# Kernel tuning notes

Hardware: AMD Instinct MI355X
Metric: run time of the kernel (lower is better)

The kernel has to match this reference:

```python
import jax, jax.numpy as jnp
import numpy as np

B, N, NC = 16, 25200, 80
CONF_THRES = 0.25
IOU_THRES = 0.45
MAX_DET = 300
MAX_WH = 7680.0   # yolov5 per-class box offset for class-aware NMS
TOPK = 1024       # pre-NMS candidate cap (fixed-shape stand-in for yolov5 max_nms)


def setup_inputs():
    key = jax.random.key(0)
    k1, k2 = jax.random.split(key)
    # xywh in pixel units (640x640 image, boxes up to ~120 px); obj/cls confidences in [0,1]
    xywh = jax.random.uniform(k1, (B, N, 4), dtype=jnp.float32) * jnp.array([640.0, 640.0, 120.0, 120.0], jnp.float32)
    conf = jax.random.uniform(k2, (B, N, 1 + NC), dtype=jnp.float32)
    return {"YOLOoutput": jnp.concatenate([xywh, conf], axis=-1)}


def _xywh2xyxy(x):
    cx, cy, w, h = x[..., 0], x[..., 1], x[..., 2], x[..., 3]
    return jnp.stack([cx - w / 2, cy - h / 2, cx + w / 2, cy + h / 2], axis=-1)


def _pairwise_iou(a, b):
    # a, b: [K,4] xyxy -> [K,K]
    lt = jnp.maximum(a[:, None, :2], b[None, :, :2])
    rb = jnp.minimum(a[:, None, 2:], b[None, :, 2:])
    wh = jnp.maximum(rb - lt, 0.0)
    inter = wh[..., 0] * wh[..., 1]
    area_a = (a[:, 2] - a[:, 0]) * (a[:, 3] - a[:, 1])
    area_b = (b[:, 2] - b[:, 0]) * (b[:, 3] - b[:, 1])
    return inter / (area_a[:, None] + area_b[None, :] - inter + 1e-7)


def _nms_single(pred):
    # pred: [N, 5+NC]
    obj = pred[:, 4]
    cls_conf = pred[:, 5:] * obj[:, None]      # conf = obj_conf * cls_conf (yolov5)
    conf = jnp.max(cls_conf, axis=-1)
    j = jnp.argmax(cls_conf, axis=-1)
    valid = (obj > CONF_THRES) & (conf > CONF_THRES)
    box = _xywh2xyxy(pred[:, :4])
    scores = jnp.where(valid, conf, -1.0)      # invalid candidates sink to bottom
    top_scores, idx = jax.lax.top_k(scores, TOPK)
    b = box[idx]                               # [TOPK,4]
    c = j[idx].astype(box.dtype)
    boxes_off = b + (c * MAX_WH)[:, None]      # class-aware NMS via per-class offset
    valid_k = top_scores > 0.0
    iou = _pairwise_iou(boxes_off, boxes_off)
    ar = jnp.arange(TOPK)

    def body(i, supp):
        active = jnp.logical_not(supp[i])
        return supp | (active & (iou[i] > IOU_THRES) & (ar > i))

    supp = jax.lax.fori_loop(0, TOPK, body, jnp.logical_not(valid_k))
    keep = valid_k & jnp.logical_not(supp)
    fs, fi = jax.lax.top_k(jnp.where(keep, top_scores, -1.0), MAX_DET)
    dv = fs > 0.0
    det_box = b[fi] * dv[:, None]              # zero out padded rows
    det = jnp.concatenate(
        [det_box, jnp.where(dv, fs, 0.0)[:, None], (c[fi] * dv)[:, None]], axis=-1
    )                                          # [MAX_DET, 6] = x1,y1,x2,y2,conf,cls
    return det, dv


def reference(YOLOoutput):
    det, dvalid = jax.vmap(_nms_single)(YOLOoutput)   # [B,MAX_DET,6], [B,MAX_DET]
    scores = det[..., 4]
    mean_conf = jnp.max(scores, axis=1)               # = 0 when image has no detections
    n = dvalid.sum(axis=1)
    terms = jnp.abs(det[..., 0:2] - det[..., 2:4]) * scores[..., None]  # padded rows are 0
    s = terms.sum(axis=(1, 2))
    wh = jnp.where(n > 0, s / (2.0 * jnp.maximum(n, 1)), 0.0)  # mean over n*2 elements
    conf_addition = mean_conf.sum() / B
    w_and_h = wh.sum() / B
    return conf_addition, w_and_h, det[2]
```

## Files before the change

kernel.cpp:

```cpp
#include <hip/hip_runtime.h>
#include <hip/hip_bf16.h>

typedef unsigned long long u64;
typedef unsigned int u32;

#define BATCH 16
#define NANCH 25200
#define NCLS 80
#define NFEAT 85
#define TOPK 1024
#define MAXDET 300
#define CONF_T 0.25f
#define IOU_T 0.45f
#define MAX_WH 7680.0f

#define TILE_A 64

__device__ __forceinline__ void gload_lds16(const void* g, void* l) {
    __builtin_amdgcn_global_load_lds(
        (const __attribute__((address_space(1))) unsigned int*)g,
        (__attribute__((address_space(3))) unsigned int*)l, 16, 0, 0);
}

__global__ __launch_bounds__(256) void score_kernel(const float* __restrict__ in,
                                                    u64* __restrict__ keys) {
    __shared__ float ld[TILE_A * NFEAT];
    const int b = blockIdx.y, tid = threadIdx.x;
    const int wv = tid >> 6, lane = tid & 63;
    const int a0 = blockIdx.x * TILE_A;
    const int na = min(TILE_A, NANCH - a0);
    const int nbytes = na * NFEAT * 4;
    const char* gbase = (const char*)(in + ((size_t)b * NANCH + a0) * NFEAT);
#pragma unroll
    for (int r = 0; r < 6; ++r) {
        const int off = (r * 4 + wv) << 10;
        const int myb = off + lane * 16;
        if (myb < nbytes)
            gload_lds16(gbase + myb, (char*)ld + off);
    }
    __syncthreads();
    const int a = tid >> 2, q = tid & 3;
    if (a < na) {
        const float* p = ld + a * NFEAT;
        float obj = p[4];
        float best = -1e30f;
        int bj = 0;
#pragma unroll
        for (int k = 0; k < 20; ++k) {
            float v = p[5 + q * 20 + k] * obj;
            if (v > best) { best = v; bj = q * 20 + k; }
        }
#pragma unroll
        for (int d = 1; d < 4; d <<= 1) {
            float ob = __shfl_xor(best, d, 64);
            int oj = __shfl_xor(bj, d, 64);
            if (ob > best || (ob == best && oj < bj)) { best = ob; bj = oj; }
        }
        if (q == 0) {
            bool valid = (obj > CONF_T) && (best > CONF_T);
            float sc = valid ? best : -1.0f;
            u32 sb = __float_as_uint(sc);
            u32 ord = sb ^ ((sb & 0x80000000u) ? 0xFFFFFFFFu : 0x80000000u);
            int idx = a0 + a;
            keys[(size_t)b * NANCH + idx] =
                ((u64)ord << 32) | ((u64)((u32)(idx ^ 0xFFFF) & 0xFFFFu) << 8) | (u64)bj;
        }
    }
}

__global__ __launch_bounds__(1024) void select_topk(const u64* __restrict__ keys,
                                                    const float* __restrict__ in,
                                                    float4* __restrict__ box4,
                                                    float4* __restrict__ boxoff4,
                                                    float* __restrict__ score,
                                                    float* __restrict__ cls,
                                                    u64* __restrict__ vmask,
                                                    float* __restrict__ out) {
    const int b = blockIdx.x, tid = threadIdx.x;
    const int lane = tid & 63, wv = tid >> 6;
    const u64* kb = keys + (size_t)b * NANCH;
    __shared__ u32 hist[4096];
    __shared__ u32 wtot[16];
    __shared__ u32 wsfx[16];
    __shared__ u32 s_prefix12, s_cnt;
    __shared__ u64 buf[2048];

    if (b == 0 && tid == 0) { out[0] = 0.0f; out[1] = 0.0f; }

#pragma unroll
    for (int i = 0; i < 4; ++i) hist[tid * 4 + i] = 0u;
    __syncthreads();
#pragma unroll 4
    for (int n = tid; n < NANCH; n += 1024) {
        u32 hi = (u32)(kb[n] >> 32);
        atomicAdd(&hist[hi >> 20], 1u);
    }
    __syncthreads();
    u32 h0 = hist[tid * 4], h1 = hist[tid * 4 + 1];
    u32 h2 = hist[tid * 4 + 2], h3 = hist[tid * 4 + 3];
    u32 s3v = h3, s2v = h2 + s3v, s1v = h1 + s2v, s0v = h0 + s1v;
    u32 S = s0v;
#pragma unroll
    for (int d = 1; d < 64; d <<= 1) {
        u32 o = __shfl_down(S, d, 64);
        if (lane + d < 64) S += o;
    }
    if (lane == 0) wtot[wv] = S;
    __syncthreads();
    if (tid == 0) {
        u32 acc = 0;
        for (int w = 15; w >= 0; --w) { wsfx[w] = acc; acc += wtot[w]; }
    }
    __syncthreads();
    {
        const u32 E = wsfx[wv] + (S - s0v);
        const u32 v0 = E + s0v, v1 = E + s1v, v2 = E + s2v, v3 = E + s3v, v4 = E;
        if (v0 >= (u32)TOPK && v1 < (u32)TOPK) s_prefix12 = (u32)(tid * 4 + 0);
        if (v1 >= (u32)TOPK && v2 < (u32)TOPK) s_prefix12 = (u32)(tid * 4 + 1);
        if (v2 >= (u32)TOPK && v3 < (u32)TOPK) s_prefix12 = (u32)(tid * 4 + 2);
        if (v3 >= (u32)TOPK && v4 < (u32)TOPK) s_prefix12 = (u32)(tid * 4 + 3);
    }
    if (tid == 0) s_cnt = 0u;
    __syncthreads();
    const u32 p12 = s_prefix12;
#pragma unroll 4
    for (int n = tid; n < NANCH; n += 1024) {
        u64 k = kb[n];
        if (((u32)(k >> 32) >> 20) > p12) {
            u32 pos = atomicAdd(&s_cnt, 1u);
            if (pos < 2048u) buf[pos] = k;
        }
    }
    __syncthreads();
#pragma unroll 4
    for (int n = tid; n < NANCH; n += 1024) {
        u64 k = kb[n];
        if (((u32)(k >> 32) >> 20) == p12) {
            u32 pos = atomicAdd(&s_cnt, 1u);
            if (pos < 2048u) buf[pos] = k;
        }
    }
    __syncthreads();
    u32 cnt = s_cnt; if (cnt > 2048u) cnt = 2048u;
    for (int n = (int)cnt + tid; n < 2048; n += 1024) buf[n] = 0ull;
    __syncthreads();

    const int base = wv * 128;
    u64 r0 = buf[base + lane], r1 = buf[base + 64 + lane];
    for (int k2 = 2; k2 <= 128; k2 <<= 1) {
        const bool d0 = (((base + lane) & k2) == 0);
        const bool d1 = (((base + 64 + lane) & k2) == 0);
        for (int jj = (k2 >> 1); jj >= 1; jj >>= 1) {
            if (jj == 64) {
                u64 mx = r0 > r1 ? r0 : r1, mn = r0 > r1 ? r1 : r0;
                r0 = d0 ? mx : mn; r1 = d0 ? mn : mx;
            } else {
                const bool up = (lane & jj) != 0;
                u64 v0 = __shfl_xor(r0, jj, 64);
                u64 v1 = __shfl_xor(r1, jj, 64);
                const bool km0 = (d0 != up), km1 = (d1 != up);
                r0 = km0 ? (r0 > v0 ? r0 : v0) : (r0 < v0 ? r0 : v0);
                r1 = km1 ? (r1 > v1 ? r1 : v1) : (r1 < v1 ? r1 : v1);
            }
        }
    }
    for (int k2 = 256; k2 <= 2048; k2 <<= 1) {
        buf[base + lane] = r0; buf[base + 64 + lane] = r1;
        __syncthreads();
        for (int jj = (k2 >> 1); jj >= 128; jj >>= 1) {
            int i = ((tid & ~(jj - 1)) << 1) | (tid & (jj - 1));
            int part = i | jj;
            u64 a = buf[i], c = buf[part];
            bool sw = ((i & k2) == 0) ? (a < c) : (a > c);
            if (sw) { buf[i] = c; buf[part] = a; }
            __syncthreads();
        }
        r0 = buf[base + lane]; r1 = buf[base + 64 + lane];
        const bool d0 = (((base + lane) & k2) == 0);
        for (int jj = 64; jj >= 1; jj >>= 1) {
            if (jj == 64) {
                u64 mx = r0 > r1 ? r0 : r1, mn = r0 > r1 ? r1 : r0;
                r0 = d0 ? mx : mn; r1 = d0 ? mn : mx;
            } else {
                const bool up = (lane & jj) != 0;
                u64 v0 = __shfl_xor(r0, jj, 64);
                u64 v1 = __shfl_xor(r1, jj, 64);
                const bool km = (d0 != up);
                r0 = km ? (r0 > v0 ? r0 : v0) : (r0 < v0 ? r0 : v0);
                r1 = km ? (r1 > v1 ? r1 : v1) : (r1 < v1 ? r1 : v1);
            }
        }
    }
    buf[base + lane] = r0; buf[base + 64 + lane] = r1;
    __syncthreads();

    u64 k = buf[tid];
    u32 ord = (u32)(k >> 32);
    u32 sb = (ord & 0x80000000u) ? (ord ^ 0x80000000u) : ~ord;
    float sc = __uint_as_float(sb);
    int idx = (int)((((u32)(k >> 8)) & 0xFFFFu) ^ 0xFFFFu);
    int j = (int)(k & 0xFFu);
    const float* pr = in + ((size_t)b * NANCH + idx) * NFEAT;
    float cx = pr[0], cy = pr[1], ww = pr[2], hh = pr[3];
    float x1 = cx - ww / 2.0f, y1 = cy - hh / 2.0f;
    float x2 = cx + ww / 2.0f, y2 = cy + hh / 2.0f;
    float c = (float)j;
    float cm = c * MAX_WH;
    box4[b * TOPK + tid]    = make_float4(x1, y1, x2, y2);
    boxoff4[b * TOPK + tid] = make_float4(x1 + cm, y1 + cm, x2 + cm, y2 + cm);
    score[b * TOPK + tid] = sc;
    cls[b * TOPK + tid] = c;
    u64 bal = __ballot(sc > 0.0f);
    if ((tid & 63) == 0) vmask[b * 16 + (tid >> 6)] = bal;
}

__global__ __launch_bounds__(256) void iou_mask(const float4* __restrict__ boxoff4,
                                                u64* __restrict__ M) {
    __shared__ float4 sbx[TOPK];
    const int b = blockIdx.x >> 8;
    const int rb = blockIdx.x & 255;
    const int i = (rb << 2) | (threadIdx.x >> 6);
    const int lane = threadIdx.x & 63;
    const int tw = rb >> 4;
    const int jmin = tw << 6;
    for (int t = jmin + threadIdx.x; t < TOPK; t += 256) sbx[t] = boxoff4[b * TOPK + t];
    __syncthreads();
    const float4 A = sbx[i];
    const float areaA = (A.z - A.x) * (A.w - A.y);
    u64 myword = 0ull;
#pragma unroll 4
    for (int t = tw; t < 16; ++t) {
        int j = (t << 6) | lane;
        float4 Bx = sbx[j];
        float lx = fmaxf(A.x, Bx.x), ly = fmaxf(A.y, Bx.y);
        float rx = fminf(A.z, Bx.z), ry = fminf(A.w, Bx.w);
        float iw = fmaxf(rx - lx, 0.0f), ih = fmaxf(ry - ly, 0.0f);
        float inter = iw * ih;
        float areaB = (Bx.z - Bx.x) * (Bx.w - Bx.y);
        float iou = inter / (areaA + areaB - inter + 1e-7f);
        bool pred = (iou > IOU_T) && (j > i);
        u64 bal = __ballot(pred);
        if (lane == t) myword = bal;
    }
    if (lane < 16) M[((size_t)b * TOPK + i) * 16 + lane] = myword;
}

__global__ __launch_bounds__(512) void nms_finalize(const u64* __restrict__ M,
                                                    const u64* __restrict__ vmask,
                                                    const float4* __restrict__ box4,
                                                    const float* __restrict__ score,
                                                    const float* __restrict__ cls,
                                                    float* __restrict__ out) {
    __shared__ u64 sM[TOPK * 16];
    __shared__ u64 kw[16];
    __shared__ int wpfx[17];
    __shared__ float sdet[MAXDET * 6];
    __shared__ float s_sum, s_max;
    const int b = blockIdx.x, tid = threadIdx.x;
    {
        const ulonglong2* Ms = (const ulonglong2*)(M + (size_t)b * TOPK * 16);
        ulonglong2* Ldst = (ulonglong2*)sM;
#pragma unroll 4
        for (int t = tid; t < TOPK * 8; t += 512) Ldst[t] = Ms[t];
    }
    for (int t = tid; t < MAXDET * 6; t += 512) sdet[t] = 0.0f;
    if (tid == 0) { s_sum = 0.0f; s_max = 0.0f; }
    __syncthreads();
    if (tid < 16) {
        const int w = tid;
        const u64 vm = vmask[b * 16 + w];
        u64 supp = ~vm;
        u64 rwA[16], rwB[16];
#pragma unroll
        for (int q = 0; q < 16; ++q) rwA[q] = sM[q * 16 + w];
        for (int wb = 0; wb < 16; ++wb) {
            u64 cur = __shfl(supp, wb, 64);
#pragma unroll
            for (int c4 = 0; c4 < 4; ++c4) {
                const int rn = wb * 64 + (c4 + 1) * 16;
                if (rn < 1024) {
#pragma unroll
                    for (int q = 0; q < 16; ++q) rwB[q] = sM[(rn + q) * 16 + w];
                }
                u64 rc[16];
#pragma unroll
                for (int q = 0; q < 16; ++q) rc[q] = __shfl(rwA[q], wb, 64);
                u64 ar0 = rc[0] | rc[4] | rc[8]  | rc[12];
                u64 ar1 = rc[1] | rc[5] | rc[9]  | rc[13];
                u64 ar2 = rc[2] | rc[6] | rc[10] | rc[14];
                u64 ar3 = rc[3] | rc[7] | rc[11] | rc[15];
                const u32 intra = (u32)(((ar0 | ar1) | (ar2 | ar3)) >> (c4 * 16)) & 0xFFFFu;
                const u32 actm  = (~(u32)(cur >> (c4 * 16))) & 0xFFFFu;
                if (intra == 0u || actm == 0u) {
                    u64 s0 = 0, s1 = 0, s2 = 0, s3 = 0;
                    u64 c0 = 0, c1 = 0, c2 = 0, c3 = 0;
#pragma unroll
                    for (int q = 0; q < 16; q += 4) {
                        const u64 m0 = ((actm >> (q + 0)) & 1u) ? ~0ull : 0ull;
                        const u64 m1 = ((actm >> (q + 1)) & 1u) ? ~0ull : 0ull;
                        const u64 m2 = ((actm >> (q + 2)) & 1u) ? ~0ull : 0ull;
                        const u64 m3 = ((actm >> (q + 3)) & 1u) ? ~0ull : 0ull;
                        s0 |= rwA[q + 0] & m0;  c0 |= rc[q + 0] & m0;
                        s1 |= rwA[q + 1] & m1;  c1 |= rc[q + 1] & m1;
                        s2 |= rwA[q + 2] & m2;  c2 |= rc[q + 2] & m2;
                        s3 |= rwA[q + 3] & m3;  c3 |= rc[q + 3] & m3;
                    }
                    supp |= (s0 | s1) | (s2 | s3);
                    cur  |= (c0 | c1) | (c2 | c3);
                } else {
#pragma unroll
                    for (int q = 0; q < 16; ++q) {
                        const int ii = c4 * 16 + q;
                        const bool act = ((cur >> ii) & 1ull) == 0ull;
                        supp = act ? (supp | rwA[q]) : supp;
                        cur  = act ? (cur  | rc[q])  : cur;
                    }
                }
#pragma unroll
                for (int q = 0; q < 16; ++q) rwA[q] = rwB[q];
            }
        }
        kw[w] = vm & ~supp;
    }
    __syncthreads();
    if (tid == 0) {
        int acc = 0;
        for (int w = 0; w < 16; ++w) { wpfx[w] = acc; acc += __popcll(kw[w]); }
        wpfx[16] = acc;
    }
    __syncthreads();
    for (int r = tid; r < TOPK; r += 512) {
        int w = r >> 6, bp = r & 63;
        if ((kw[w] >> bp) & 1ull) {
            int pos = wpfx[w] + __popcll(kw[w] & ((1ull << bp) - 1ull));
            if (pos < MAXDET) {
                float4 bx = box4[b * TOPK + r];
                float s = score[b * TOPK + r];
                float c = cls[b * TOPK + r];
                sdet[pos * 6 + 0] = bx.x;
                sdet[pos * 6 + 1] = bx.y;
                sdet[pos * 6 + 2] = bx.z;
                sdet[pos * 6 + 3] = bx.w;
                sdet[pos * 6 + 4] = s;
                sdet[pos * 6 + 5] = c;
                float term = (fabsf(bx.x - bx.z) + fabsf(bx.y - bx.w)) * s;
                atomicAdd(&s_sum, term);
                if (pos == 0) s_max = s;
            }
        }
    }
    __syncthreads();
    if (tid == 0) {
        int n = wpfx[16]; if (n > MAXDET) n = MAXDET;
        float wh = (n > 0) ? (s_sum / (2.0f * (float)n)) : 0.0f;
        atomicAdd(&out[0], s_max / (float)BATCH);
        atomicAdd(&out[1], wh / (float)BATCH);
    }
    if (b == 2) {
        for (int t = tid; t < MAXDET * 6; t += 512) out[2 + t] = sdet[t];
    }
}

extern "C" void kernel_launch(void* const* d_in, const int* in_sizes, int n_in,
                              void* d_out, int out_size, void* d_ws, size_t ws_size,
                              hipStream_t stream) {
    const float* in = (const float*)d_in[0];
    float* out = (float*)d_out;
    char* ws = (char*)d_ws;

    u64*    keys     = (u64*)   (ws + 0);
    float4* boxoff4  = (float4*)(ws + 3225600);
    float4* box4     = (float4*)(ws + 3487744);
    float*  score    = (float*) (ws + 3749888);
    float*  cls      = (float*) (ws + 3815424);
    u64*    vmask    = (u64*)   (ws + 3880960);
    u64*    M        = (u64*)   (ws + 3883008);

    score_kernel<<<dim3(394, BATCH), 256, 0, stream>>>(in, keys);
    select_topk<<<BATCH, 1024, 0, stream>>>(keys, in, box4, boxoff4, score, cls, vmask, out);
    iou_mask<<<BATCH * 256, 256, 0, stream>>>(boxoff4, M);
    nms_finalize<<<BATCH, 512, 0, stream>>>(M, vmask, box4, score, cls, out);
}
```

Before: 275.8 us.

## Fuse top-k selection, IoU mask and NMS finalize into one per-batch kernel

```diff
diff --git a/kernel.cpp b/kernel.cpp
--- a/kernel.cpp
+++ b/kernel.cpp
@@ -23,10 +23,12 @@
 }
 
 __global__ __launch_bounds__(256) void score_kernel(const float* __restrict__ in,
-                                                    u64* __restrict__ keys) {
+                                                    u64* __restrict__ keys,
+                                                    float* __restrict__ out) {
     __shared__ float ld[TILE_A * NFEAT];
     const int b = blockIdx.y, tid = threadIdx.x;
     const int wv = tid >> 6, lane = tid & 63;
+    if (blockIdx.x == 0 && b == 0 && tid == 0) { out[0] = 0.0f; out[1] = 0.0f; }
     const int a0 = blockIdx.x * TILE_A;
     const int na = min(TILE_A, NANCH - a0);
     const int nbytes = na * NFEAT * 4;
@@ -68,25 +70,31 @@
     }
 }
 
-__global__ __launch_bounds__(1024) void select_topk(const u64* __restrict__ keys,
+__global__ __launch_bounds__(1024) void fused_batch(const u64* __restrict__ keys,
                                                     const float* __restrict__ in,
-                                                    float4* __restrict__ box4,
-                                                    float4* __restrict__ boxoff4,
-                                                    float* __restrict__ score,
-                                                    float* __restrict__ cls,
-                                                    u64* __restrict__ vmask,
                                                     float* __restrict__ out) {
+    __shared__ u64 sM[TOPK * 16];
+    __shared__ float4 sbox[TOPK];
+    __shared__ float sscore[TOPK];
+    __shared__ unsigned char sclsa[TOPK];
+    __shared__ u64 kwv[16];
+    __shared__ u64 kw[16];
+    __shared__ int wpfx[17];
+    __shared__ u32 wtot[16];
+    __shared__ u32 wsfx[16];
+    __shared__ u32 s_prefix12, s_cnt;
+    __shared__ float s_sum, s_max;
+    u32* hist = (u32*)sM;
+    u64* buf  = sM + 2048;
+
     const int b = blockIdx.x, tid = threadIdx.x;
     const int lane = tid & 63, wv = tid >> 6;
     const u64* kb = keys + (size_t)b * NANCH;
-    __shared__ u32 hist[4096];
-    __shared__ u32 wtot[16];
-    __shared__ u32 wsfx[16];
-    __shared__ u32 s_prefix12, s_cnt;
-    __shared__ u64 buf[2048];
-
-    if (b == 0 && tid == 0) { out[0] = 0.0f; out[1] = 0.0f; }
-
+
+    if (b == 2) {
+        for (int t = tid; t < MAXDET * 6; t += 1024) out[2 + t] = 0.0f;
+    }
+    if (tid == 0) { s_sum = 0.0f; s_max = 0.0f; s_cnt = 0u; }
 #pragma unroll
     for (int i = 0; i < 4; ++i) hist[tid * 4 + i] = 0u;
     __syncthreads();
@@ -120,7 +128,6 @@
         if (v2 >= (u32)TOPK && v3 < (u32)TOPK) s_prefix12 = (u32)(tid * 4 + 2);
         if (v3 >= (u32)TOPK && v4 < (u32)TOPK) s_prefix12 = (u32)(tid * 4 + 3);
     }
-    if (tid == 0) s_cnt = 0u;
     __syncthreads();
     const u32 p12 = s_prefix12;
 #pragma unroll 4
@@ -145,130 +152,122 @@
     for (int n = (int)cnt + tid; n < 2048; n += 1024) buf[n] = 0ull;
     __syncthreads();
 
-    const int base = wv * 128;
-    u64 r0 = buf[base + lane], r1 = buf[base + 64 + lane];
-    for (int k2 = 2; k2 <= 128; k2 <<= 1) {
-        const bool d0 = (((base + lane) & k2) == 0);
-        const bool d1 = (((base + 64 + lane) & k2) == 0);
-        for (int jj = (k2 >> 1); jj >= 1; jj >>= 1) {
-            if (jj == 64) {
-                u64 mx = r0 > r1 ? r0 : r1, mn = r0 > r1 ? r1 : r0;
-                r0 = d0 ? mx : mn; r1 = d0 ? mn : mx;
-            } else {
-                const bool up = (lane & jj) != 0;
-                u64 v0 = __shfl_xor(r0, jj, 64);
-                u64 v1 = __shfl_xor(r1, jj, 64);
-                const bool km0 = (d0 != up), km1 = (d1 != up);
-                r0 = km0 ? (r0 > v0 ? r0 : v0) : (r0 < v0 ? r0 : v0);
-                r1 = km1 ? (r1 > v1 ? r1 : v1) : (r1 < v1 ? r1 : v1);
-            }
-        }
-    }
-    for (int k2 = 256; k2 <= 2048; k2 <<= 1) {
+    {
+        const int base = wv * 128;
+        u64 r0 = buf[base + lane], r1 = buf[base + 64 + lane];
+        for (int k2 = 2; k2 <= 128; k2 <<= 1) {
+            const bool d0 = (((base + lane) & k2) == 0);
+            const bool d1 = (((base + 64 + lane) & k2) == 0);
+            for (int jj = (k2 >> 1); jj >= 1; jj >>= 1) {
+                if (jj == 64) {
+                    u64 mx = r0 > r1 ? r0 : r1, mn = r0 > r1 ? r1 : r0;
+                    r0 = d0 ? mx : mn; r1 = d0 ? mn : mx;
+                } else {
+                    const bool up = (lane & jj) != 0;
+                    u64 v0 = __shfl_xor(r0, jj, 64);
+                    u64 v1 = __shfl_xor(r1, jj, 64);
+                    const bool km0 = (d0 != up), km1 = (d1 != up);
+                    r0 = km0 ? (r0 > v0 ? r0 : v0) : (r0 < v0 ? r0 : v0);
+                    r1 = km1 ? (r1 > v1 ? r1 : v1) : (r1 < v1 ? r1 : v1);
+                }
+            }
+        }
+        for (int k2 = 256; k2 <= 2048; k2 <<= 1) {
+            buf[base + lane] = r0; buf[base + 64 + lane] = r1;
+            __syncthreads();
+            for (int jj = (k2 >> 1); jj >= 128; jj >>= 1) {
+                int i = ((tid & ~(jj - 1)) << 1) | (tid & (jj - 1));
+                int part = i | jj;
+                u64 a = buf[i], c = buf[part];
+                bool sw = ((i & k2) == 0) ? (a < c) : (a > c);
+                if (sw) { buf[i] = c; buf[part] = a; }
+                __syncthreads();
+            }
+            r0 = buf[base + lane]; r1 = buf[base + 64 + lane];
+            const bool d0 = (((base + lane) & k2) == 0);
+            for (int jj = 64; jj >= 1; jj >>= 1) {
+                if (jj == 64) {
+                    u64 mx = r0 > r1 ? r0 : r1, mn = r0 > r1 ? r1 : r0;
+                    r0 = d0 ? mx : mn; r1 = d0 ? mn : mx;
+                } else {
+                    const bool up = (lane & jj) != 0;
+                    u64 v0 = __shfl_xor(r0, jj, 64);
+                    u64 v1 = __shfl_xor(r1, jj, 64);
+                    const bool km = (d0 != up);
+                    r0 = km ? (r0 > v0 ? r0 : v0) : (r0 < v0 ? r0 : v0);
+                    r1 = km ? (r1 > v1 ? r1 : v1) : (r1 < v1 ? r1 : v1);
+                }
+            }
+        }
         buf[base + lane] = r0; buf[base + 64 + lane] = r1;
-        __syncthreads();
-        for (int jj = (k2 >> 1); jj >= 128; jj >>= 1) {
-            int i = ((tid & ~(jj - 1)) << 1) | (tid & (jj - 1));
-            int part = i | jj;
-            u64 a = buf[i], c = buf[part];
-            bool sw = ((i & k2) == 0) ? (a < c) : (a > c);
-            if (sw) { buf[i] = c; buf[part] = a; }
-            __syncthreads();
-        }
-        r0 = buf[base + lane]; r1 = buf[base + 64 + lane];
-        const bool d0 = (((base + lane) & k2) == 0);
-        for (int jj = 64; jj >= 1; jj >>= 1) {
-            if (jj == 64) {
-                u64 mx = r0 > r1 ? r0 : r1, mn = r0 > r1 ? r1 : r0;
-                r0 = d0 ? mx : mn; r1 = d0 ? mn : mx;
-            } else {
-                const bool up = (lane & jj) != 0;
-                u64 v0 = __shfl_xor(r0, jj, 64);
-                u64 v1 = __shfl_xor(r1, jj, 64);
-                const bool km = (d0 != up);
-                r0 = km ? (r0 > v0 ? r0 : v0) : (r0 < v0 ? r0 : v0);
-                r1 = km ? (r1 > v1 ? r1 : v1) : (r1 < v1 ? r1 : v1);
-            }
-        }
-    }
-    buf[base + lane] = r0; buf[base + 64 + lane] = r1;
-    __syncthreads();
-
-    u64 k = buf[tid];
-    u32 ord = (u32)(k >> 32);
-    u32 sb = (ord & 0x80000000u) ? (ord ^ 0x80000000u) : ~ord;
-    float sc = __uint_as_float(sb);
-    int idx = (int)((((u32)(k >> 8)) & 0xFFFFu) ^ 0xFFFFu);
-    int j = (int)(k & 0xFFu);
-    const float* pr = in + ((size_t)b * NANCH + idx) * NFEAT;
-    float cx = pr[0], cy = pr[1], ww = pr[2], hh = pr[3];
-    float x1 = cx - ww / 2.0f, y1 = cy - hh / 2.0f;
-    float x2 = cx + ww / 2.0f, y2 = cy + hh / 2.0f;
-    float c = (float)j;
-    float cm = c * MAX_WH;
-    box4[b * TOPK + tid]    = make_float4(x1, y1, x2, y2);
-    boxoff4[b * TOPK + tid] = make_float4(x1 + cm, y1 + cm, x2 + cm, y2 + cm);
-    score[b * TOPK + tid] = sc;
-    cls[b * TOPK + tid] = c;
-    u64 bal = __ballot(sc > 0.0f);
-    if ((tid & 63) == 0) vmask[b * 16 + (tid >> 6)] = bal;
-}
-
-__global__ __launch_bounds__(256) void iou_mask(const float4* __restrict__ boxoff4,
-                                                u64* __restrict__ M) {
-    __shared__ float4 sbx[TOPK];
-    const int b = blockIdx.x >> 8;
-    const int rb = blockIdx.x & 255;
-    const int i = (rb << 2) | (threadIdx.x >> 6);
-    const int lane = threadIdx.x & 63;
-    const int tw = rb >> 4;
-    const int jmin = tw << 6;
-    for (int t = jmin + threadIdx.x; t < TOPK; t += 256) sbx[t] = boxoff4[b * TOPK + t];
-    __syncthreads();
-    const float4 A = sbx[i];
-    const float areaA = (A.z - A.x) * (A.w - A.y);
-    u64 myword = 0ull;
-#pragma unroll 4
-    for (int t = tw; t < 16; ++t) {
-        int j = (t << 6) | lane;
-        float4 Bx = sbx[j];
-        float lx = fmaxf(A.x, Bx.x), ly = fmaxf(A.y, Bx.y);
-        float rx = fminf(A.z, Bx.z), ry = fminf(A.w, Bx.w);
-        float iw = fmaxf(rx - lx, 0.0f), ih = fmaxf(ry - ly, 0.0f);
-        float inter = iw * ih;
-        float areaB = (Bx.z - Bx.x) * (Bx.w - Bx.y);
-        float iou = inter / (areaA + areaB - inter + 1e-7f);
-        bool pred = (iou > IOU_T) && (j > i);
-        u64 bal = __ballot(pred);
-        if (lane == t) myword = bal;
-    }
-    if (lane < 16) M[((size_t)b * TOPK + i) * 16 + lane] = myword;
-}
-
-__global__ __launch_bounds__(512) void nms_finalize(const u64* __restrict__ M,
-                                                    const u64* __restrict__ vmask,
-                                                    const float4* __restrict__ box4,
-                                                    const float* __restrict__ score,
-                                                    const float* __restrict__ cls,
-                                                    float* __restrict__ out) {
-    __shared__ u64 sM[TOPK * 16];
-    __shared__ u64 kw[16];
-    __shared__ int wpfx[17];
-    __shared__ float sdet[MAXDET * 6];
-    __shared__ float s_sum, s_max;
-    const int b = blockIdx.x, tid = threadIdx.x;
-    {
-        const ulonglong2* Ms = (const ulonglong2*)(M + (size_t)b * TOPK * 16);
-        ulonglong2* Ldst = (ulonglong2*)sM;
-#pragma unroll 4
-        for (int t = tid; t < TOPK * 8; t += 512) Ldst[t] = Ms[t];
-    }
-    for (int t = tid; t < MAXDET * 6; t += 512) sdet[t] = 0.0f;
-    if (tid == 0) { s_sum = 0.0f; s_max = 0.0f; }
-    __syncthreads();
+    }
+    __syncthreads();
+
+    {
+        u64 k = buf[tid];
+        u32 ord = (u32)(k >> 32);
+        u32 sb = (ord & 0x80000000u) ? (ord ^ 0x80000000u) : ~ord;
+        float sc = __uint_as_float(sb);
+        int idx = (int)((((u32)(k >> 8)) & 0xFFFFu) ^ 0xFFFFu);
+        int j = (int)(k & 0xFFu);
+        const float* pr = in + ((size_t)b * NANCH + idx) * NFEAT;
+        float cx = pr[0], cy = pr[1], ww = pr[2], hh = pr[3];
+        float x1 = cx - ww / 2.0f, y1 = cy - hh / 2.0f;
+        float x2 = cx + ww / 2.0f, y2 = cy + hh / 2.0f;
+        sbox[tid] = make_float4(x1, y1, x2, y2);
+        sscore[tid] = sc;
+        sclsa[tid] = (unsigned char)j;
+        u64 bal = __ballot(sc > 0.0f);
+        if (lane == 0) kwv[wv] = bal;
+    }
+    __syncthreads();
+
+    {
+        float4 Bo[16]; float areaB[16]; u32 Bcls[16];
+#pragma unroll
+        for (int t = 0; t < 16; ++t) {
+            const int j2 = (t << 6) | lane;
+            const float4 p = sbox[j2];
+            const u32 cj = (u32)sclsa[j2];
+            const float cm = (float)cj * MAX_WH;
+            const float bx1 = p.x + cm, by1 = p.y + cm;
+            const float bx2 = p.z + cm, by2 = p.w + cm;
+            Bo[t] = make_float4(bx1, by1, bx2, by2);
+            areaB[t] = (bx2 - bx1) * (by2 - by1);
+            Bcls[t] = cj;
+        }
+        for (int r = 0; r < 64; ++r) {
+            const int i = (r << 4) | wv;
+            const int tw = i >> 6;
+            const float4 a = sbox[i];
+            const u32 ci = (u32)sclsa[i];
+            const float acm = (float)ci * MAX_WH;
+            const float ax1 = a.x + acm, ay1 = a.y + acm;
+            const float ax2 = a.z + acm, ay2 = a.w + acm;
+            const float areaA = (ax2 - ax1) * (ay2 - ay1);
+            u64 myword = 0ull;
+#pragma unroll
+            for (int t = 0; t < 16; ++t) {
+                if (t < tw) continue;
+                if (__ballot(Bcls[t] == ci) == 0ull) continue;
+                float lx = fmaxf(ax1, Bo[t].x), ly = fmaxf(ay1, Bo[t].y);
+                float rx = fminf(ax2, Bo[t].z), ry = fminf(ay2, Bo[t].w);
+                float iw = fmaxf(rx - lx, 0.0f), ih = fmaxf(ry - ly, 0.0f);
+                float inter = iw * ih;
+                float iou = inter / (areaA + areaB[t] - inter + 1e-7f);
+                const int j = (t << 6) | lane;
+                bool pred = (iou > IOU_T) && (j > i);
+                u64 bal = __ballot(pred);
+                if (lane == t) myword = bal;
+            }
+            if (lane < 16) sM[i * 16 + lane] = myword;
+        }
+    }
+    __syncthreads();
+
     if (tid < 16) {
         const int w = tid;
-        const u64 vm = vmask[b * 16 + w];
+        const u64 vm = kwv[w];
         u64 supp = ~vm;
         u64 rwA[16], rwB[16];
 #pragma unroll
@@ -329,23 +328,27 @@
         wpfx[16] = acc;
     }
     __syncthreads();
-    for (int r = tid; r < TOPK; r += 512) {
-        int w = r >> 6, bp = r & 63;
+
+    {
+        const int r = tid;
+        const int w = r >> 6, bp = r & 63;
         if ((kw[w] >> bp) & 1ull) {
             int pos = wpfx[w] + __popcll(kw[w] & ((1ull << bp) - 1ull));
             if (pos < MAXDET) {
-                float4 bx = box4[b * TOPK + r];
-                float s = score[b * TOPK + r];
-                float c = cls[b * TOPK + r];
-                sdet[pos * 6 + 0] = bx.x;
-                sdet[pos * 6 + 1] = bx.y;
-                sdet[pos * 6 + 2] = bx.z;
-                sdet[pos * 6 + 3] = bx.w;
-                sdet[pos * 6 + 4] = s;
-                sdet[pos * 6 + 5] = c;
+                float4 bx = sbox[r];
+                float s = sscore[r];
+                float c = (float)sclsa[r];
                 float term = (fabsf(bx.x - bx.z) + fabsf(bx.y - bx.w)) * s;
                 atomicAdd(&s_sum, term);
                 if (pos == 0) s_max = s;
+                if (b == 2) {
+                    out[2 + pos * 6 + 0] = bx.x;
+                    out[2 + pos * 6 + 1] = bx.y;
+                    out[2 + pos * 6 + 2] = bx.z;
+                    out[2 + pos * 6 + 3] = bx.w;
+                    out[2 + pos * 6 + 4] = s;
+                    out[2 + pos * 6 + 5] = c;
+                }
             }
         }
     }
@@ -355,9 +358,6 @@
         float wh = (n > 0) ? (s_sum / (2.0f * (float)n)) : 0.0f;
         atomicAdd(&out[0], s_max / (float)BATCH);
         atomicAdd(&out[1], wh / (float)BATCH);
-    }
-    if (b == 2) {
-        for (int t = tid; t < MAXDET * 6; t += 512) out[2 + t] = sdet[t];
     }
 }
 
@@ -368,16 +368,8 @@
     float* out = (float*)d_out;
     char* ws = (char*)d_ws;
 
-    u64*    keys     = (u64*)   (ws + 0);
-    float4* boxoff4  = (float4*)(ws + 3225600);
-    float4* box4     = (float4*)(ws + 3487744);
-    float*  score    = (float*) (ws + 3749888);
-    float*  cls      = (float*) (ws + 3815424);
-    u64*    vmask    = (u64*)   (ws + 3880960);
-    u64*    M        = (u64*)   (ws + 3883008);
-
-    score_kernel<<<dim3(394, BATCH), 256, 0, stream>>>(in, keys);
-    select_topk<<<BATCH, 1024, 0, stream>>>(keys, in, box4, boxoff4, score, cls, vmask, out);
-    iou_mask<<<BATCH * 256, 256, 0, stream>>>(boxoff4, M);
-    nms_finalize<<<BATCH, 512, 0, stream>>>(M, vmask, box4, score, cls, out);
+    u64* keys = (u64*)(ws + 0);
+
+    score_kernel<<<dim3(394, BATCH), 256, 0, stream>>>(in, keys, out);
+    fused_batch<<<BATCH, 1024, 0, stream>>>(keys, in, out);
 }
```

New measurement: 353.9 us. 28.3% more time.

## Split top-k selection into histogram, threshold, grid-wide compaction and sort kernels

Applied to the files above, without the earlier changes.

```diff
diff --git a/kernel.cpp b/kernel.cpp
--- a/kernel.cpp
+++ b/kernel.cpp
@@ -22,11 +22,19 @@
         (__attribute__((address_space(3))) unsigned int*)l, 16, 0, 0);
 }
 
+__global__ __launch_bounds__(1024) void zero_hist(u32* __restrict__ z) {
+    const int t = blockIdx.x * 1024 + threadIdx.x;
+    if (t < 65584) z[t] = 0u;
+}
+
 __global__ __launch_bounds__(256) void score_kernel(const float* __restrict__ in,
-                                                    u64* __restrict__ keys) {
+                                                    u64* __restrict__ keys,
+                                                    u32* __restrict__ hist,
+                                                    float* __restrict__ out) {
     __shared__ float ld[TILE_A * NFEAT];
     const int b = blockIdx.y, tid = threadIdx.x;
     const int wv = tid >> 6, lane = tid & 63;
+    if (blockIdx.x == 0 && b == 0 && tid == 0) { out[0] = 0.0f; out[1] = 0.0f; }
     const int a0 = blockIdx.x * TILE_A;
     const int na = min(TILE_A, NANCH - a0);
     const int nbytes = na * NFEAT * 4;
@@ -64,40 +72,22 @@
             int idx = a0 + a;
             keys[(size_t)b * NANCH + idx] =
                 ((u64)ord << 32) | ((u64)((u32)(idx ^ 0xFFFF) & 0xFFFFu) << 8) | (u64)bj;
-        }
-    }
-}
-
-__global__ __launch_bounds__(1024) void select_topk(const u64* __restrict__ keys,
-                                                    const float* __restrict__ in,
-                                                    float4* __restrict__ box4,
-                                                    float4* __restrict__ boxoff4,
-                                                    float* __restrict__ score,
-                                                    float* __restrict__ cls,
-                                                    u64* __restrict__ vmask,
-                                                    float* __restrict__ out) {
+            u64 ibal = __ballot(!valid);
+            if (valid) atomicAdd(&hist[b * 4096 + (ord >> 20)], 1u);
+            if (lane == 0 && ibal) atomicAdd(&hist[b * 4096 + 0x407], (u32)__popcll(ibal));
+        }
+    }
+}
+
+__global__ __launch_bounds__(1024) void select_threshold(const u32* __restrict__ hist,
+                                                         u32* __restrict__ p12arr) {
     const int b = blockIdx.x, tid = threadIdx.x;
     const int lane = tid & 63, wv = tid >> 6;
-    const u64* kb = keys + (size_t)b * NANCH;
-    __shared__ u32 hist[4096];
-    __shared__ u32 wtot[16];
-    __shared__ u32 wsfx[16];
-    __shared__ u32 s_prefix12, s_cnt;
-    __shared__ u64 buf[2048];
-
-    if (b == 0 && tid == 0) { out[0] = 0.0f; out[1] = 0.0f; }
-
-#pragma unroll
-    for (int i = 0; i < 4; ++i) hist[tid * 4 + i] = 0u;
-    __syncthreads();
-#pragma unroll 4
-    for (int n = tid; n < NANCH; n += 1024) {
-        u32 hi = (u32)(kb[n] >> 32);
-        atomicAdd(&hist[hi >> 20], 1u);
-    }
-    __syncthreads();
-    u32 h0 = hist[tid * 4], h1 = hist[tid * 4 + 1];
-    u32 h2 = hist[tid * 4 + 2], h3 = hist[tid * 4 + 3];
+    __shared__ u32 wtot[16], wsfx[16];
+    __shared__ u32 s_prefix12;
+    const u32* hb = hist + b * 4096;
+    u32 h0 = hb[tid * 4], h1 = hb[tid * 4 + 1];
+    u32 h2 = hb[tid * 4 + 2], h3 = hb[tid * 4 + 3];
     u32 s3v = h3, s2v = h2 + s3v, s1v = h1 + s2v, s0v = h0 + s1v;
     u32 S = s0v;
 #pragma unroll
@@ -120,29 +110,66 @@
         if (v2 >= (u32)TOPK && v3 < (u32)TOPK) s_prefix12 = (u32)(tid * 4 + 2);
         if (v3 >= (u32)TOPK && v4 < (u32)TOPK) s_prefix12 = (u32)(tid * 4 + 3);
     }
-    if (tid == 0) s_cnt = 0u;
-    __syncthreads();
-    const u32 p12 = s_prefix12;
-#pragma unroll 4
-    for (int n = tid; n < NANCH; n += 1024) {
-        u64 k = kb[n];
-        if (((u32)(k >> 32) >> 20) > p12) {
-            u32 pos = atomicAdd(&s_cnt, 1u);
-            if (pos < 2048u) buf[pos] = k;
-        }
-    }
-    __syncthreads();
-#pragma unroll 4
-    for (int n = tid; n < NANCH; n += 1024) {
-        u64 k = kb[n];
-        if (((u32)(k >> 32) >> 20) == p12) {
-            u32 pos = atomicAdd(&s_cnt, 1u);
-            if (pos < 2048u) buf[pos] = k;
-        }
-    }
-    __syncthreads();
-    u32 cnt = s_cnt; if (cnt > 2048u) cnt = 2048u;
-    for (int n = (int)cnt + tid; n < 2048; n += 1024) buf[n] = 0ull;
+    __syncthreads();
+    if (tid == 0) p12arr[b] = s_prefix12;
+}
+
+__global__ __launch_bounds__(256) void compact(const u64* __restrict__ keys,
+                                               const u32* __restrict__ p12arr,
+                                               u32* __restrict__ cA, u32* __restrict__ cE,
+                                               u64* __restrict__ bufA, u64* __restrict__ bufE) {
+    const int b = blockIdx.y;
+    const int n = blockIdx.x * 256 + threadIdx.x;
+    const int lane = threadIdx.x & 63;
+    const u32 p12 = p12arr[b];
+    u64 k = 0ull; bool haveA = false, haveE = false;
+    if (n < NANCH) {
+        k = keys[(size_t)b * NANCH + n];
+        const u32 pfx = (u32)(k >> 52);
+        haveA = pfx > p12; haveE = pfx == p12;
+    }
+    const u64 balA = __ballot(haveA);
+    const u64 balE = __ballot(haveE);
+    u32 baseA = 0, baseE = 0;
+    if (lane == 0) {
+        if (balA) baseA = atomicAdd(&cA[b], (u32)__popcll(balA));
+        if (balE) baseE = atomicAdd(&cE[b], (u32)__popcll(balE));
+    }
+    baseA = __shfl(baseA, 0, 64);
+    baseE = __shfl(baseE, 0, 64);
+    const u64 lmask = (1ull << lane) - 1ull;
+    if (haveA) {
+        u32 pos = baseA + (u32)__popcll(balA & lmask);
+        if (pos < 1024u) bufA[b * 1024 + pos] = k;
+    }
+    if (haveE) {
+        u32 pos = baseE + (u32)__popcll(balE & lmask);
+        if (pos < 3072u) bufE[b * 3072 + pos] = k;
+    }
+}
+
+__global__ __launch_bounds__(1024) void sort_extract(const u64* __restrict__ bufA,
+                                                     const u64* __restrict__ bufE,
+                                                     const u32* __restrict__ cA,
+                                                     const u32* __restrict__ cE,
+                                                     const float* __restrict__ in,
+                                                     float4* __restrict__ box4,
+                                                     float4* __restrict__ boxoff4,
+                                                     float* __restrict__ score,
+                                                     float* __restrict__ cls,
+                                                     u64* __restrict__ vmask) {
+    __shared__ u64 buf[2048];
+    const int b = blockIdx.x, tid = threadIdx.x;
+    const int lane = tid & 63, wv = tid >> 6;
+    const u32 nA = min(cA[b], 1024u);
+    const u32 nE = min(min(cE[b], 3072u), 2048u - nA);
+#pragma unroll
+    for (int t = tid; t < 2048; t += 1024) {
+        u64 v = 0ull;
+        if (t < (int)nA) v = bufA[b * 1024 + t];
+        else if (t - (int)nA < (int)nE) v = bufE[b * 3072 + (t - (int)nA)];
+        buf[t] = v;
+    }
     __syncthreads();
 
     const int base = wv * 128;
@@ -375,9 +402,19 @@
     float*  cls      = (float*) (ws + 3815424);
     u64*    vmask    = (u64*)   (ws + 3880960);
     u64*    M        = (u64*)   (ws + 3883008);
-
-    score_kernel<<<dim3(394, BATCH), 256, 0, stream>>>(in, keys);
-    select_topk<<<BATCH, 1024, 0, stream>>>(keys, in, box4, boxoff4, score, cls, vmask, out);
+    u32*    hist     = (u32*)   (ws + 3883008);
+    u32*    p12arr   = (u32*)   (ws + 4145152);
+    u32*    cntA     = (u32*)   (ws + 4145216);
+    u32*    cntE     = (u32*)   (ws + 4145280);
+    u64*    bufA     = (u64*)   (ws + 4145344);
+    u64*    bufE     = (u64*)   (ws + 4276416);
+
+    zero_hist<<<65, 1024, 0, stream>>>(hist);
+    score_kernel<<<dim3(394, BATCH), 256, 0, stream>>>(in, keys, hist, out);
+    select_threshold<<<BATCH, 1024, 0, stream>>>(hist, p12arr);
+    compact<<<dim3(99, BATCH), 256, 0, stream>>>(keys, p12arr, cntA, cntE, bufA, bufE);
+    sort_extract<<<BATCH, 1024, 0, stream>>>(bufA, bufE, cntA, cntE, in, box4, boxoff4,
+                                             score, cls, vmask);
     iou_mask<<<BATCH * 256, 256, 0, stream>>>(boxoff4, M);
     nms_finalize<<<BATCH, 512, 0, stream>>>(M, vmask, box4, score, cls, out);
 }
```

Result: slower. 413.1 us (+49.8%).

## Make score kernel persistent with per-wave 16-anchor groups and no block barrier

Applied to the files above, without the earlier changes.

```diff
diff --git a/kernel.cpp b/kernel.cpp
--- a/kernel.cpp
+++ b/kernel.cpp
@@ -14,7 +14,9 @@
 #define IOU_T 0.45f
 #define MAX_WH 7680.0f
 
-#define TILE_A 64
+#define GRP 16
+#define GRPB (GRP * NFEAT * 4)
+#define NGRP (NANCH / GRP)
 
 __device__ __forceinline__ void gload_lds16(const void* g, void* l) {
     __builtin_amdgcn_global_load_lds(
@@ -23,31 +25,33 @@
 }
 
 __global__ __launch_bounds__(256) void score_kernel(const float* __restrict__ in,
-                                                    u64* __restrict__ keys) {
-    __shared__ float ld[TILE_A * NFEAT];
-    const int b = blockIdx.y, tid = threadIdx.x;
-    const int wv = tid >> 6, lane = tid & 63;
-    const int a0 = blockIdx.x * TILE_A;
-    const int na = min(TILE_A, NANCH - a0);
-    const int nbytes = na * NFEAT * 4;
-    const char* gbase = (const char*)(in + ((size_t)b * NANCH + a0) * NFEAT);
-#pragma unroll
-    for (int r = 0; r < 6; ++r) {
-        const int off = (r * 4 + wv) << 10;
-        const int myb = off + lane * 16;
-        if (myb < nbytes)
-            gload_lds16(gbase + myb, (char*)ld + off);
-    }
-    __syncthreads();
-    const int a = tid >> 2, q = tid & 3;
-    if (a < na) {
-        const float* p = ld + a * NFEAT;
-        float obj = p[4];
+                                                    u64* __restrict__ keys,
+                                                    float* __restrict__ out) {
+    __shared__ char lds[4 * GRPB];
+    const int tid = threadIdx.x, wv = tid >> 6, lane = tid & 63;
+    if (blockIdx.x == 0 && tid == 0) { out[0] = 0.0f; out[1] = 0.0f; }
+    char* myl = lds + wv * GRPB;
+    const float* myp = (const float*)myl + (lane >> 2) * NFEAT;
+    const int a = lane >> 2, q = lane & 3;
+    const int wave_id = (blockIdx.x << 2) | wv;
+    const int nwaves = gridDim.x << 2;
+    for (int g = wave_id; g < BATCH * NGRP; g += nwaves) {
+        const int b = g / NGRP;
+        const int a0 = (g - b * NGRP) * GRP;
+        const char* gbase = (const char*)(in + ((size_t)b * NANCH + a0) * NFEAT);
+#pragma unroll
+        for (int r = 0; r < 6; ++r) {
+            const int myb = (r << 10) + lane * 16;
+            if (myb < GRPB) gload_lds16(gbase + myb, myl + (r << 10));
+        }
+        asm volatile("s_waitcnt vmcnt(0)" ::: "memory");
+        __builtin_amdgcn_sched_barrier(0);
+        float obj = myp[4];
         float best = -1e30f;
         int bj = 0;
 #pragma unroll
         for (int k = 0; k < 20; ++k) {
-            float v = p[5 + q * 20 + k] * obj;
+            float v = myp[5 + q * 20 + k] * obj;
             if (v > best) { best = v; bj = q * 20 + k; }
         }
 #pragma unroll
@@ -74,8 +78,7 @@
                                                     float4* __restrict__ boxoff4,
                                                     float* __restrict__ score,
                                                     float* __restrict__ cls,
-                                                    u64* __restrict__ vmask,
-                                                    float* __restrict__ out) {
+                                                    u64* __restrict__ vmask) {
     const int b = blockIdx.x, tid = threadIdx.x;
     const int lane = tid & 63, wv = tid >> 6;
     const u64* kb = keys + (size_t)b * NANCH;
@@ -84,8 +87,6 @@
     __shared__ u32 wsfx[16];
     __shared__ u32 s_prefix12, s_cnt;
     __shared__ u64 buf[2048];
-
-    if (b == 0 && tid == 0) { out[0] = 0.0f; out[1] = 0.0f; }
 
 #pragma unroll
     for (int i = 0; i < 4; ++i) hist[tid * 4 + i] = 0u;
@@ -376,8 +377,8 @@
     u64*    vmask    = (u64*)   (ws + 3880960);
     u64*    M        = (u64*)   (ws + 3883008);
 
-    score_kernel<<<dim3(394, BATCH), 256, 0, stream>>>(in, keys);
-    select_topk<<<BATCH, 1024, 0, stream>>>(keys, in, box4, boxoff4, score, cls, vmask, out);
+    score_kernel<<<2048, 256, 0, stream>>>(in, keys, out);
+    select_topk<<<BATCH, 1024, 0, stream>>>(keys, in, box4, boxoff4, score, cls, vmask);
     iou_mask<<<BATCH * 256, 256, 0, stream>>>(boxoff4, M);
     nms_finalize<<<BATCH, 512, 0, stream>>>(M, vmask, box4, score, cls, out);
 }
```

Result: no change. 278.2 us (+0.9%).
